# Performance work log

Measured on AMD Instinct MI355X. Metric: run time of the kernel, lower is better.

Reference implementation:

```python
import jax, jax.numpy as jnp
import numpy as np

BOUND = 1.0
GRID = 128
DENSITY_SCALE = 1.0
DENSITY_THRESH = 0.01
T_THRESH = 1e-3
BG_COLOR = 1.0
N_RAYS = 65536
N_STEPS = 128


def setup_inputs() -> dict:
    key = jax.random.key(0)
    ks = jax.random.split(key, 7)
    N, S = N_RAYS, N_STEPS
    # ray origins inside the AABB, directions unit-norm
    rays_o = (jax.random.uniform(ks[0], (N, 3)) - 0.5) * 1.0
    d = jax.random.normal(ks[1], (N, 3))
    rays_d = d / jnp.linalg.norm(d, axis=-1, keepdims=True)
    sigmas = jax.random.uniform(ks[2], (N, S)) * 2.0      # raw densities at samples
    rgbs = jax.random.uniform(ks[3], (N, S, 3))           # albedo at samples
    sun_v = jax.random.uniform(ks[4], (N, S))             # sun visibility (shadow)
    sky_color = jax.random.uniform(ks[5], (N, S, 3))      # ambient sky color
    nears = jnp.full((N,), 0.2, dtype=jnp.float32)
    fars = jnp.full((N,), 2.0, dtype=jnp.float32)
    density_grid = jax.random.uniform(ks[6], (GRID, GRID, GRID))  # occupancy grid
    return dict(rays_o=rays_o, rays_d=rays_d, sigmas=sigmas, rgbs=rgbs,
                sun_v=sun_v, sky_color=sky_color, nears=nears, fars=fars,
                density_grid=density_grid)


def reference(rays_o, rays_d, sigmas, rgbs, sun_v, sky_color, nears, fars, density_grid):
    N, S = sigmas.shape
    # --- march: uniform samples in [near, far] (dt_gamma = 0) ---
    dt = (fars - nears) / S                                        # [N]
    t = nears[:, None] + (jnp.arange(S, dtype=sigmas.dtype) + 0.5) * dt[:, None]  # [N,S]
    xyz = rays_o[:, None, :] + t[..., None] * rays_d[:, None, :]   # [N,S,3]
    # --- occupancy-grid lookup (density_bitfield test) ---
    idx = jnp.clip(((xyz + BOUND) / (2.0 * BOUND) * GRID).astype(jnp.int32), 0, GRID - 1)
    occ = density_grid[idx[..., 0], idx[..., 1], idx[..., 2]] > DENSITY_THRESH  # [N,S]
    inside = jnp.all(jnp.abs(xyz) < BOUND, axis=-1)                # AABB clip
    sig = jnp.where(occ & inside, sigmas * DENSITY_SCALE, 0.0)     # skip empty space
    # --- shading: irradiance = sun_v + (1 - sun_v) * sky_color ---
    irr = sun_v[..., None] + (1.0 - sun_v[..., None]) * sky_color  # [N,S,3]
    rgb = rgbs * irr
    # --- alpha compositing with early termination ---
    tau = sig * dt[:, None]                                        # optical depth per step
    T = jnp.exp(-(jnp.cumsum(tau, axis=-1) - tau))                 # exclusive transmittance
    alpha = 1.0 - jnp.exp(-tau)
    w = jnp.where(T > T_THRESH, alpha * T, 0.0)                    # early-termination mask
    weights_sum = w.sum(-1)                                        # [N]
    depth = (w * t).sum(-1)                                        # [N]
    image = jnp.einsum('ns,nsc->nc', w, rgb) + (1.0 - weights_sum)[:, None] * BG_COLOR
    depth = jnp.clip(depth - nears, 0.0) / (fars - nears)
    return image, depth, weights_sum
```

## Files before the change

### kernel.cpp

```cpp
#include <hip/hip_runtime.h>


#define NRAYS  65536
#define NSTEPS 128
#define GRIDN  128

typedef float v2f __attribute__((ext_vector_type(2)));

__global__ __launch_bounds__(256, 4) void nerf_render_kernel(
    const float* __restrict__ rays_o,
    const float* __restrict__ rays_d,
    const float* __restrict__ sigmas,
    const float* __restrict__ rgbs,
    const float* __restrict__ sun_v,
    const float* __restrict__ sky,
    const float* __restrict__ nears,
    const float* __restrict__ fars,
    const float* __restrict__ grid,
    float* __restrict__ out)
{
    const int tid  = blockIdx.x * blockDim.x + threadIdx.x;
    const int ray  = tid >> 6;
    const int lane = threadIdx.x & 63;
    if (ray >= NRAYS) return;

    const float nearv = nears[ray];
    const float farv  = fars[ray];
    const float dt    = (farv - nearv) * (1.0f / NSTEPS);

    const float ox = rays_o[ray * 3 + 0];
    const float oy = rays_o[ray * 3 + 1];
    const float oz = rays_o[ray * 3 + 2];
    const float dx = rays_d[ray * 3 + 0];
    const float dy = rays_d[ray * 3 + 1];
    const float dz = rays_d[ray * 3 + 2];

    const int  s0   = 2 * lane;
    const long base = (long)ray * NSTEPS + s0;

    const v2f sg = __builtin_nontemporal_load((const v2f*)(sigmas + base));
    const v2f sv = __builtin_nontemporal_load((const v2f*)(sun_v  + base));
    const v2f r01 = __builtin_nontemporal_load((const v2f*)(rgbs + base * 3));
    const v2f r23 = __builtin_nontemporal_load((const v2f*)(rgbs + base * 3 + 2));
    const v2f r45 = __builtin_nontemporal_load((const v2f*)(rgbs + base * 3 + 4));
    const v2f k01 = __builtin_nontemporal_load((const v2f*)(sky  + base * 3));
    const v2f k23 = __builtin_nontemporal_load((const v2f*)(sky  + base * 3 + 2));
    const v2f k45 = __builtin_nontemporal_load((const v2f*)(sky  + base * 3 + 4));

    float t_[2], tau_[2], cr_[2], cg_[2], cb_[2];
    const float rr_[2] = { r01[0], r23[1] };
    const float rg_[2] = { r01[1], r45[0] };
    const float rb_[2] = { r23[0], r45[1] };
    const float kr_[2] = { k01[0], k23[1] };
    const float kg_[2] = { k01[1], k45[0] };
    const float kb_[2] = { k23[0], k45[1] };

    #pragma unroll
    for (int j = 0; j < 2; ++j) {
        const int s = s0 + j;
        const float t = __fadd_rn(nearv, __fmul_rn((float)s + 0.5f, dt));
        const float x = __fadd_rn(ox, __fmul_rn(t, dx));
        const float y = __fadd_rn(oy, __fmul_rn(t, dy));
        const float z = __fadd_rn(oz, __fmul_rn(t, dz));

        int ix = (int)__fmul_rn(__fadd_rn(x, 1.0f), 64.0f);
        int iy = (int)__fmul_rn(__fadd_rn(y, 1.0f), 64.0f);
        int iz = (int)__fmul_rn(__fadd_rn(z, 1.0f), 64.0f);
        ix = min(max(ix, 0), GRIDN - 1);
        iy = min(max(iy, 0), GRIDN - 1);
        iz = min(max(iz, 0), GRIDN - 1);
        const float g = grid[((long)ix * GRIDN + iy) * GRIDN + iz];

        const bool inside = (fabsf(x) < 1.0f) & (fabsf(y) < 1.0f) & (fabsf(z) < 1.0f);
        const bool occ    = (g > 0.01f) & inside;

        const float sig = occ ? sg[j] : 0.0f;

        const float s_v = sv[j];
        cr_[j] = rr_[j] * (s_v + (1.0f - s_v) * kr_[j]);
        cg_[j] = rg_[j] * (s_v + (1.0f - s_v) * kg_[j]);
        cb_[j] = rb_[j] * (s_v + (1.0f - s_v) * kb_[j]);

        t_[j]   = t;
        tau_[j] = sig * dt;
    }

    const float pair = tau_[0] + tau_[1];
    float incl = pair;
    #pragma unroll
    for (int off = 1; off < 64; off <<= 1) {
        const float u = __shfl_up(incl, off);
        if (lane >= off) incl += u;
    }
    const float eLane = incl - pair;
    const float excl_[2] = { eLane, eLane + tau_[0] };

    float wsum = 0.0f, dsum = 0.0f, ir = 0.0f, ig = 0.0f, ib = 0.0f;
    #pragma unroll
    for (int j = 0; j < 2; ++j) {
        const float T     = expf(-excl_[j]);
        const float alpha = 1.0f - expf(-tau_[j]);
        const float w     = (T > 1e-3f) ? alpha * T : 0.0f;
        wsum += w; dsum += w * t_[j];
        ir += w * cr_[j]; ig += w * cg_[j]; ib += w * cb_[j];
    }

    #pragma unroll
    for (int off = 32; off > 0; off >>= 1) {
        wsum += __shfl_xor(wsum, off);
        dsum += __shfl_xor(dsum, off);
        ir   += __shfl_xor(ir, off);
        ig   += __shfl_xor(ig, off);
        ib   += __shfl_xor(ib, off);
    }

    if (lane == 0) {
        const float bgw = 1.0f - wsum;
        out[ray * 3 + 0] = ir + bgw;
        out[ray * 3 + 1] = ig + bgw;
        out[ray * 3 + 2] = ib + bgw;
        out[3 * NRAYS + ray] = fmaxf(dsum - nearv, 0.0f) / (farv - nearv);
        out[4 * NRAYS + ray] = wsum;
    }
}

extern "C" void kernel_launch(void* const* d_in, const int* in_sizes, int n_in,
                              void* d_out, int out_size, void* d_ws, size_t ws_size,
                              hipStream_t stream) {
    const float* rays_o = (const float*)d_in[0];
    const float* rays_d = (const float*)d_in[1];
    const float* sigmas = (const float*)d_in[2];
    const float* rgbs   = (const float*)d_in[3];
    const float* sun_v  = (const float*)d_in[4];
    const float* sky    = (const float*)d_in[5];
    const float* nears  = (const float*)d_in[6];
    const float* fars   = (const float*)d_in[7];
    const float* grid   = (const float*)d_in[8];
    float* out = (float*)d_out;

    const int threads = 256;
    const int blocks  = (NRAYS * 64) / threads;
    nerf_render_kernel<<<blocks, threads, 0, stream>>>(
        rays_o, rays_d, sigmas, rgbs, sun_v, sky, nears, fars, grid, out);
}
```

Measured before the change: 298.7 us.

## Process two rays per wavefront with four samples per lane and 128-bit loads

Remaps work so each 64-lane wavefront handles two rays, each half-wave covering 128 samples with four samples per lane loaded via 16-byte vector loads. The scan and reduction shrink from 6 to 5 shuffle steps and launch fewer threads, which cuts per-sample shuffle and index overhead. Each lane now does more serial work and holds more registers, and the bounds check on ray was removed.

```diff
diff --git a/kernel.cpp b/kernel.cpp
--- a/kernel.cpp
+++ b/kernel.cpp
@@ -5,7 +5,7 @@
 #define NSTEPS 128
 #define GRIDN  128
 
-typedef float v2f __attribute__((ext_vector_type(2)));
+typedef float v4f __attribute__((ext_vector_type(4)));
 
 __global__ __launch_bounds__(256, 4) void nerf_render_kernel(
     const float* __restrict__ rays_o,
@@ -20,9 +20,11 @@
     float* __restrict__ out)
 {
     const int tid  = blockIdx.x * blockDim.x + threadIdx.x;
-    const int ray  = tid >> 6;
+    const int wave = tid >> 6;
     const int lane = threadIdx.x & 63;
-    if (ray >= NRAYS) return;
+    const int half = lane >> 5;
+    const int l32  = lane & 31;
+    const int ray  = wave * 2 + half;
 
     const float nearv = nears[ray];
     const float farv  = fars[ray];
@@ -35,28 +37,29 @@
     const float dy = rays_d[ray * 3 + 1];
     const float dz = rays_d[ray * 3 + 2];
 
-    const int  s0   = 2 * lane;
+    const int  s0   = 4 * l32;
     const long base = (long)ray * NSTEPS + s0;
 
-    const v2f sg = __builtin_nontemporal_load((const v2f*)(sigmas + base));
-    const v2f sv = __builtin_nontemporal_load((const v2f*)(sun_v  + base));
-    const v2f r01 = __builtin_nontemporal_load((const v2f*)(rgbs + base * 3));
-    const v2f r23 = __builtin_nontemporal_load((const v2f*)(rgbs + base * 3 + 2));
-    const v2f r45 = __builtin_nontemporal_load((const v2f*)(rgbs + base * 3 + 4));
-    const v2f k01 = __builtin_nontemporal_load((const v2f*)(sky  + base * 3));
-    const v2f k23 = __builtin_nontemporal_load((const v2f*)(sky  + base * 3 + 2));
-    const v2f k45 = __builtin_nontemporal_load((const v2f*)(sky  + base * 3 + 4));
+    const v4f sg = __builtin_nontemporal_load((const v4f*)(sigmas + base));
+    const v4f sv = __builtin_nontemporal_load((const v4f*)(sun_v  + base));
+    const v4f r0 = __builtin_nontemporal_load((const v4f*)(rgbs + base * 3));
+    const v4f r1 = __builtin_nontemporal_load((const v4f*)(rgbs + base * 3 + 4));
+    const v4f r2 = __builtin_nontemporal_load((const v4f*)(rgbs + base * 3 + 8));
+    const v4f k0 = __builtin_nontemporal_load((const v4f*)(sky  + base * 3));
+    const v4f k1 = __builtin_nontemporal_load((const v4f*)(sky  + base * 3 + 4));
+    const v4f k2 = __builtin_nontemporal_load((const v4f*)(sky  + base * 3 + 8));
 
-    float t_[2], tau_[2], cr_[2], cg_[2], cb_[2];
-    const float rr_[2] = { r01[0], r23[1] };
-    const float rg_[2] = { r01[1], r45[0] };
-    const float rb_[2] = { r23[0], r45[1] };
-    const float kr_[2] = { k01[0], k23[1] };
-    const float kg_[2] = { k01[1], k45[0] };
-    const float kb_[2] = { k23[0], k45[1] };
+    const float rr_[4] = { r0[0], r0[3], r1[2], r2[1] };
+    const float rg_[4] = { r0[1], r1[0], r1[3], r2[2] };
+    const float rb_[4] = { r0[2], r1[1], r2[0], r2[3] };
+    const float kr_[4] = { k0[0], k0[3], k1[2], k2[1] };
+    const float kg_[4] = { k0[1], k1[0], k1[3], k2[2] };
+    const float kb_[4] = { k0[2], k1[1], k2[0], k2[3] };
+
+    float t_[4], tau_[4], cr_[4], cg_[4], cb_[4];
 
     #pragma unroll
-    for (int j = 0; j < 2; ++j) {
+    for (int j = 0; j < 4; ++j) {
         const int s = s0 + j;
         const float t = __fadd_rn(nearv, __fmul_rn((float)s + 0.5f, dt));
         const float x = __fadd_rn(ox, __fmul_rn(t, dx));
@@ -85,28 +88,28 @@
         tau_[j] = sig * dt;
     }
 
-    const float pair = tau_[0] + tau_[1];
-    float incl = pair;
+    const float tot = tau_[0] + tau_[1] + tau_[2] + tau_[3];
+    float incl = tot;
     #pragma unroll
-    for (int off = 1; off < 64; off <<= 1) {
+    for (int off = 1; off < 32; off <<= 1) {
         const float u = __shfl_up(incl, off);
-        if (lane >= off) incl += u;
+        if (l32 >= off) incl += u;
     }
-    const float eLane = incl - pair;
-    const float excl_[2] = { eLane, eLane + tau_[0] };
+    float run = incl - tot;
 
     float wsum = 0.0f, dsum = 0.0f, ir = 0.0f, ig = 0.0f, ib = 0.0f;
     #pragma unroll
-    for (int j = 0; j < 2; ++j) {
-        const float T     = expf(-excl_[j]);
+    for (int j = 0; j < 4; ++j) {
+        const float T     = expf(-run);
         const float alpha = 1.0f - expf(-tau_[j]);
         const float w     = (T > 1e-3f) ? alpha * T : 0.0f;
         wsum += w; dsum += w * t_[j];
         ir += w * cr_[j]; ig += w * cg_[j]; ib += w * cb_[j];
+        run += tau_[j];
     }
 
     #pragma unroll
-    for (int off = 32; off > 0; off >>= 1) {
+    for (int off = 16; off > 0; off >>= 1) {
         wsum += __shfl_xor(wsum, off);
         dsum += __shfl_xor(dsum, off);
         ir   += __shfl_xor(ir, off);
@@ -114,7 +117,7 @@
         ib   += __shfl_xor(ib, off);
     }
 
-    if (lane == 0) {
+    if (l32 == 0) {
         const float bgw = 1.0f - wsum;
         out[ray * 3 + 0] = ir + bgw;
         out[ray * 3 + 1] = ig + bgw;
@@ -139,7 +142,7 @@
     float* out = (float*)d_out;
 
     const int threads = 256;
-    const int blocks  = (NRAYS * 64) / threads;
+    const int blocks  = NRAYS / 8;
     nerf_render_kernel<<<blocks, threads, 0, stream>>>(
         rays_o, rays_d, sigmas, rgbs, sun_v, sky, nears, fars, grid, out);
 }
```

Result: slower. 314.0 us (+5.1%).
